# Performance work log

Measured on AMD Instinct MI355X. Metric: run time of the kernel, lower is better.

## Reference

```python
import jax, jax.numpy as jnp
import numpy as np

N_NODES = 10000
D_IN = 128
D_OUT = 128
N_EDGES = 640000


def setup_inputs() -> dict:
    key = jax.random.key(0)
    k_x, k_e, k_wl, k_wr, k_b = jax.random.split(key, 5)
    x = jax.random.normal(k_x, (N_NODES, D_IN), dtype=jnp.float32)
    edge_index = jax.random.randint(k_e, (2, N_EDGES), 0, N_NODES, dtype=jnp.int64)
    # SAGEConv params: lin_l (neighbor path, with bias), lin_r (root path, no bias)
    s_l = 1.0 / np.sqrt(D_IN)
    W_l = jax.random.uniform(k_wl, (D_OUT, D_IN), dtype=jnp.float32, minval=-s_l, maxval=s_l)
    b_l = jax.random.uniform(k_b, (D_OUT,), dtype=jnp.float32, minval=-s_l, maxval=s_l)
    W_r = jax.random.uniform(k_wr, (D_OUT, D_IN), dtype=jnp.float32, minval=-s_l, maxval=s_l)
    return {"x": x, "edge_index": edge_index, "W_l": W_l, "b_l": b_l, "W_r": W_r}


def reference(x, edge_index, W_l, b_l, W_r):
    x = x.astype(jnp.float32)
    src, dst = edge_index[0], edge_index[1]
    # gather source features, mean-aggregate into destination nodes
    msgs = x[src]                                   # [E, D_in] irregular gather
    agg_sum = jax.ops.segment_sum(msgs, dst, num_segments=N_NODES)  # [N, D_in]
    deg = jax.ops.segment_sum(jnp.ones((src.shape[0],), dtype=x.dtype), dst,
                              num_segments=N_NODES)                 # [N]
    agg = jnp.where(deg[:, None] > 0, agg_sum / jnp.maximum(deg, 1.0)[:, None], 0.0)
    # SAGEConv: lin_l(agg) + lin_r(x)
    y = agg @ W_l.T + b_l + x @ W_r.T               # [N, D_out]
    return x + y                                     # residual add
```

## Files before the change

kernel.cpp:

```cpp
#include <hip/hip_runtime.h>

#define N_NODES 10000
#define D 128
#define N_EDGES 640000
#define NB 128
#define EPB (N_EDGES / NB)
#define SB 40
#define NPSB 250

typedef __attribute__((ext_vector_type(8))) short bf16x8;
typedef __attribute__((ext_vector_type(4))) float f32x4;
typedef __attribute__((ext_vector_type(8))) unsigned short us8;
typedef __attribute__((ext_vector_type(8))) float f32x8;


__device__ __forceinline__ unsigned short f2bf(float f) {
    union { float f; unsigned int i; } v;
    v.f = f;
    unsigned int b = v.i;
    unsigned int rounded = b + 0x7fffu + ((b >> 16) & 1u);
    return (unsigned short)(rounded >> 16);
}

__device__ __forceinline__ float bf2f(unsigned short u) {
    union { unsigned int i; float f; } v;
    v.i = ((unsigned int)u) << 16;
    return v.f;
}

__device__ __forceinline__ f32x8 bf2f8(us8 v) {
    f32x8 r;
#pragma unroll
    for (int t = 0; t < 8; ++t) r[t] = bf2f(v[t]);
    return r;
}


__global__ __launch_bounds__(1024) void hist_cast_kernel(const int* __restrict__ ei,
                                                         const float4* __restrict__ x4,
                                                         const float4* __restrict__ Wl4,
                                                         const float4* __restrict__ Wr4,
                                                         ushort4* __restrict__ xh4,
                                                         ushort4* __restrict__ Wlb4,
                                                         ushort4* __restrict__ Wrb4,
                                                         unsigned short* __restrict__ lrank,
                                                         unsigned short* __restrict__ cnt,
                                                         unsigned long long* __restrict__ flags) {
    __shared__ int h[N_NODES];
    for (int n = threadIdx.x; n < N_NODES; n += 1024) h[n] = 0;
    if (blockIdx.x == 0 && threadIdx.x < SB) flags[threadIdx.x] = 0ULL;

    const int gid = blockIdx.x * 1024 + threadIdx.x;
    for (int i = gid; i < N_NODES * D / 4; i += NB * 1024) {
        float4 v = x4[i];
        ushort4 o;
        o.x = f2bf(v.x); o.y = f2bf(v.y); o.z = f2bf(v.z); o.w = f2bf(v.w);
        xh4[i] = o;
    }
    if (gid < D * D / 4) {
        float4 a = Wl4[gid], b = Wr4[gid];
        ushort4 oa, ob;
        oa.x = f2bf(a.x); oa.y = f2bf(a.y); oa.z = f2bf(a.z); oa.w = f2bf(a.w);
        ob.x = f2bf(b.x); ob.y = f2bf(b.y); ob.z = f2bf(b.z); ob.w = f2bf(b.w);
        Wlb4[gid] = oa;
        Wrb4[gid] = ob;
    }
    __syncthreads();

    const int base = blockIdx.x * EPB;
    for (int e = base + threadIdx.x; e < base + EPB; e += 1024) {
        int d = ei[N_EDGES + e];
        lrank[e] = (unsigned short)atomicAdd(&h[d], 1);
    }
    __syncthreads();
    unsigned short* c = cnt + (size_t)blockIdx.x * N_NODES;
    for (int n = threadIdx.x; n < N_NODES; n += 1024) c[n] = (unsigned short)h[n];
}


__global__ __launch_bounds__(256) void colscan_scan_kernel(unsigned short* __restrict__ cnt,
                                                           int* __restrict__ row_start,
                                                           unsigned long long* __restrict__ flags) {
    const int t = threadIdx.x;
    const int b = blockIdx.x;
    const int n = b * NPSB + t;
    __shared__ int sc[256];
    __shared__ int blk_excl_sh;

    int deg = 0;
    if (t < NPSB) {
        int s = 0;
#pragma unroll 8
        for (int j = 0; j < NB; ++j) {
            int idx = j * N_NODES + n;
            int v = cnt[idx];
            cnt[idx] = (unsigned short)s;
            s += v;
        }
        deg = s;
    }
    sc[t] = deg;
    __syncthreads();
    for (int off = 1; off < 256; off <<= 1) {
        int v = (t >= off) ? sc[t - off] : 0;
        __syncthreads();
        sc[t] += v;
        __syncthreads();
    }
    const int total = sc[255];
    const int local_excl = sc[t] - deg;

    if (t == 0) {
        int excl = 0;
        if (b == 0) {
            __hip_atomic_store(&flags[0], (2ULL << 32) | (unsigned)total,
                               __ATOMIC_RELEASE, __HIP_MEMORY_SCOPE_AGENT);
        } else {
            __hip_atomic_store(&flags[b], (1ULL << 32) | (unsigned)total,
                               __ATOMIC_RELEASE, __HIP_MEMORY_SCOPE_AGENT);
            int j = b - 1;
            while (j >= 0) {
                unsigned long long f = __hip_atomic_load(&flags[j], __ATOMIC_ACQUIRE,
                                                         __HIP_MEMORY_SCOPE_AGENT);
                unsigned st = (unsigned)(f >> 32);
                if (st == 0) continue;
                excl += (int)(unsigned)(f & 0xffffffffULL);
                if (st == 2) break;
                --j;
            }
            __hip_atomic_store(&flags[b], (2ULL << 32) | (unsigned)(excl + total),
                               __ATOMIC_RELEASE, __HIP_MEMORY_SCOPE_AGENT);
        }
        blk_excl_sh = excl;
    }
    __syncthreads();
    if (t < NPSB) row_start[n] = blk_excl_sh + local_excl;
    if (b == SB - 1 && t == 0) row_start[N_NODES] = N_EDGES;
}

__global__ __launch_bounds__(256) void scatter_kernel(const int* __restrict__ ei,
                                                      const int* __restrict__ row_start,
                                                      const unsigned short* __restrict__ cnt,
                                                      const unsigned short* __restrict__ lrank,
                                                      unsigned short* __restrict__ csr) {
    int i = blockIdx.x * 256 + threadIdx.x;
    if (i < N_EDGES) {
        int b = i / EPB;
        int s = ei[i];
        int d = ei[N_EDGES + i];
        int pos = row_start[d] + (int)cnt[b * N_NODES + d] + (int)lrank[i];
        csr[pos] = (unsigned short)s;
    }
}


__global__ __launch_bounds__(128) void aggregate_kernel(const us8* __restrict__ xh8,
                                                        const int* __restrict__ row_start,
                                                        const unsigned short* __restrict__ csr,
                                                        us8* __restrict__ aggb8) {
    __shared__ unsigned short idxs[256];
    __shared__ f32x8 red[8][16];
    const int node = blockIdx.x;
    const int lane16 = threadIdx.x & 15;
    const int slot = threadIdx.x >> 4;
    const int start = row_start[node];
    const int end = row_start[node + 1];

    f32x8 a0 = 0.f, a1 = 0.f, a2 = 0.f, a3 = 0.f;
    for (int cs = start; cs < end; cs += 256) {
        int m = min(256, end - cs);
        if ((int)threadIdx.x < m) idxs[threadIdx.x] = csr[cs + threadIdx.x];
        if ((int)threadIdx.x + 128 < m) idxs[threadIdx.x + 128] = csr[cs + threadIdx.x + 128];
        __syncthreads();
        int j = slot;
        for (; j + 24 < m; j += 32) {
            int s0 = idxs[j], s1 = idxs[j + 8], s2 = idxs[j + 16], s3 = idxs[j + 24];
            us8 v0 = xh8[s0 * 16 + lane16];
            us8 v1 = xh8[s1 * 16 + lane16];
            us8 v2 = xh8[s2 * 16 + lane16];
            us8 v3 = xh8[s3 * 16 + lane16];
            a0 += bf2f8(v0); a1 += bf2f8(v1); a2 += bf2f8(v2); a3 += bf2f8(v3);
        }
        for (; j < m; j += 8) {
            us8 v = xh8[(int)idxs[j] * 16 + lane16];
            a0 += bf2f8(v);
        }
        __syncthreads();
    }
    a0 = (a0 + a1) + (a2 + a3);
    red[slot][lane16] = a0;
    __syncthreads();
    if (slot == 0) {
        f32x8 o = red[0][lane16];
#pragma unroll
        for (int s = 1; s < 8; ++s) o += red[s][lane16];
        int cntE = end - start;
        float inv = (cntE > 0) ? 1.0f / (float)cntE : 0.0f;
        us8 pack;
#pragma unroll
        for (int t = 0; t < 8; ++t) pack[t] = f2bf(o[t] * inv);
        aggb8[node * 16 + lane16] = pack;
    }
}


__global__ __launch_bounds__(256) void lin_mfma_kernel(const float* __restrict__ x,
                                                       const unsigned short* __restrict__ aggb,
                                                       const unsigned short* __restrict__ xh,
                                                       const unsigned short* __restrict__ Wlb,
                                                       const unsigned short* __restrict__ Wrb,
                                                       const float* __restrict__ bl,
                                                       float* __restrict__ out) {
    const int wave = threadIdx.x >> 6;
    const int lane = threadIdx.x & 63;
    const int l15 = lane & 15;
    const int quad = lane >> 4;
    const int mt = blockIdx.x * 4 + wave;
    if (mt >= 625) return;
    const int row0 = mt * 16;
    const int out0 = blockIdx.y * 16;

    const int m = row0 + l15;
    const int f = out0 + l15;

    const bf16x8* arow = (const bf16x8*)(aggb + (size_t)m * D) + quad;
    const bf16x8* xrow = (const bf16x8*)(xh   + (size_t)m * D) + quad;
    const bf16x8* wlro = (const bf16x8*)(Wlb + (size_t)f * D) + quad;
    const bf16x8* wrro = (const bf16x8*)(Wrb + (size_t)f * D) + quad;

    f32x4 c = {0.f, 0.f, 0.f, 0.f};
#pragma unroll
    for (int kk = 0; kk < 4; ++kk) {
        c = __builtin_amdgcn_mfma_f32_16x16x32_bf16(arow[kk * 4], wlro[kk * 4], c, 0, 0, 0);
        c = __builtin_amdgcn_mfma_f32_16x16x32_bf16(xrow[kk * 4], wrro[kk * 4], c, 0, 0, 0);
    }

    const float bias = bl[f];
#pragma unroll
    for (int r = 0; r < 4; ++r) {
        int row = row0 + quad * 4 + r;
        int idx = row * D + f;
        out[idx] = x[idx] + bias + c[r];
    }
}

extern "C" void kernel_launch(void* const* d_in, const int* in_sizes, int n_in,
                              void* d_out, int out_size, void* d_ws, size_t ws_size,
                              hipStream_t stream) {
    const float* x  = (const float*)d_in[0];
    const int*   ei = (const int*)d_in[1];
    const float* Wl = (const float*)d_in[2];
    const float* bl = (const float*)d_in[3];
    const float* Wr = (const float*)d_in[4];
    float* out = (float*)d_out;

    unsigned long long* flags = (unsigned long long*)d_ws;
    int* row_start = (int*)(flags + 64);
    unsigned short* cnt   = (unsigned short*)(row_start + 10016);
    unsigned short* lrank = cnt + (size_t)NB * N_NODES;
    unsigned short* csr   = lrank + N_EDGES;
    unsigned short* xh    = csr + N_EDGES;
    unsigned short* aggb  = xh + (size_t)N_NODES * D;
    unsigned short* Wlb   = aggb + (size_t)N_NODES * D;
    unsigned short* Wrb   = Wlb + D * D;

    hist_cast_kernel<<<NB, 1024, 0, stream>>>(ei, (const float4*)x, (const float4*)Wl,
                                              (const float4*)Wr, (ushort4*)xh,
                                              (ushort4*)Wlb, (ushort4*)Wrb,
                                              lrank, cnt, flags);
    colscan_scan_kernel<<<SB, 256, 0, stream>>>(cnt, row_start, flags);
    scatter_kernel<<<(N_EDGES + 255) / 256, 256, 0, stream>>>(ei, row_start, cnt, lrank, csr);
    aggregate_kernel<<<N_NODES, 128, 0, stream>>>((const us8*)xh, row_start, csr,
                                                  (us8*)aggb);
    lin_mfma_kernel<<<dim3(157, 8), 256, 0, stream>>>(x, aggb, xh, Wlb, Wrb, bl, out);
}
```

Before: 121.5 us.

## Fuse all SAGE stages into one persistent kernel with grid barriers

Merges the histogram/cast, column scan, CSR scatter, mean aggregation and MFMA linear stages into a single persistent kernel of 256 blocks. The stages are separated by atomic-counter grid barriers instead of separate launches. Aggregation now maps one wave per node rather than one block per node, and reduces across slots with shuffles instead of shared memory. A memset clears the flags and barrier counter before launch. This removes launch gaps and idle tails between stages, but all blocks must be co-resident, and the per-block count array doubles in size, which makes the scan longer.

```diff
diff --git a/kernel.cpp b/kernel.cpp
--- a/kernel.cpp
+++ b/kernel.cpp
@@ -3,16 +3,17 @@
 #define N_NODES 10000
 #define D 128
 #define N_EDGES 640000
-#define NB 128
-#define EPB (N_EDGES / NB)
+#define NBLK 256
+#define NTHR 512
+#define EPB (N_EDGES / NBLK)
 #define SB 40
 #define NPSB 250
+#define NWAVES (NBLK * (NTHR / 64))
 
 typedef __attribute__((ext_vector_type(8))) short bf16x8;
 typedef __attribute__((ext_vector_type(4))) float f32x4;
 typedef __attribute__((ext_vector_type(8))) unsigned short us8;
 typedef __attribute__((ext_vector_type(8))) float f32x8;
-
 
 __device__ __forceinline__ unsigned short f2bf(float f) {
     union { float f; unsigned int i; } v;
@@ -35,212 +36,220 @@
     return r;
 }
 
-
-__global__ __launch_bounds__(1024) void hist_cast_kernel(const int* __restrict__ ei,
-                                                         const float4* __restrict__ x4,
-                                                         const float4* __restrict__ Wl4,
-                                                         const float4* __restrict__ Wr4,
-                                                         ushort4* __restrict__ xh4,
-                                                         ushort4* __restrict__ Wlb4,
-                                                         ushort4* __restrict__ Wrb4,
-                                                         unsigned short* __restrict__ lrank,
-                                                         unsigned short* __restrict__ cnt,
-                                                         unsigned long long* __restrict__ flags) {
+__device__ __forceinline__ void gbar(unsigned int* bar, unsigned int target) {
+    __syncthreads();
+    if (threadIdx.x == 0) {
+        __builtin_amdgcn_fence(__ATOMIC_RELEASE, "agent");
+        __hip_atomic_fetch_add(bar, 1u, __ATOMIC_ACQ_REL, __HIP_MEMORY_SCOPE_AGENT);
+        while (__hip_atomic_load(bar, __ATOMIC_ACQUIRE, __HIP_MEMORY_SCOPE_AGENT) < target)
+            __builtin_amdgcn_s_sleep(2);
+        __builtin_amdgcn_fence(__ATOMIC_ACQUIRE, "agent");
+    }
+    __syncthreads();
+}
+
+__global__ __launch_bounds__(NTHR) void sage_mega_kernel(
+        const float* __restrict__ x, const int* __restrict__ ei,
+        const float* __restrict__ Wl, const float* __restrict__ bl,
+        const float* __restrict__ Wr, float* __restrict__ out,
+        unsigned long long* __restrict__ flags,
+        int* __restrict__ row_start,
+        unsigned short* __restrict__ cnt,
+        unsigned short* __restrict__ lrank,
+        unsigned short* __restrict__ csr,
+        unsigned short* __restrict__ xh,
+        unsigned short* __restrict__ aggb,
+        unsigned short* __restrict__ Wlb,
+        unsigned short* __restrict__ Wrb) {
     __shared__ int h[N_NODES];
-    for (int n = threadIdx.x; n < N_NODES; n += 1024) h[n] = 0;
-    if (blockIdx.x == 0 && threadIdx.x < SB) flags[threadIdx.x] = 0ULL;
-
-    const int gid = blockIdx.x * 1024 + threadIdx.x;
-    for (int i = gid; i < N_NODES * D / 4; i += NB * 1024) {
+    unsigned int* bar = (unsigned int*)(flags + 48);
+    const int tid = threadIdx.x;
+    const int b = blockIdx.x;
+    const int gid = b * NTHR + tid;
+
+    for (int n = tid; n < N_NODES; n += NTHR) h[n] = 0;
+
+    const float4* x4 = (const float4*)x;
+    ushort4* xh4 = (ushort4*)xh;
+    for (int i = gid; i < N_NODES * D / 4; i += NBLK * NTHR) {
         float4 v = x4[i];
         ushort4 o;
         o.x = f2bf(v.x); o.y = f2bf(v.y); o.z = f2bf(v.z); o.w = f2bf(v.w);
         xh4[i] = o;
     }
     if (gid < D * D / 4) {
-        float4 a = Wl4[gid], b = Wr4[gid];
-        ushort4 oa, ob;
+        float4 a = ((const float4*)Wl)[gid], c = ((const float4*)Wr)[gid];
+        ushort4 oa, oc;
         oa.x = f2bf(a.x); oa.y = f2bf(a.y); oa.z = f2bf(a.z); oa.w = f2bf(a.w);
-        ob.x = f2bf(b.x); ob.y = f2bf(b.y); ob.z = f2bf(b.z); ob.w = f2bf(b.w);
-        Wlb4[gid] = oa;
-        Wrb4[gid] = ob;
-    }
-    __syncthreads();
-
-    const int base = blockIdx.x * EPB;
-    for (int e = base + threadIdx.x; e < base + EPB; e += 1024) {
+        oc.x = f2bf(c.x); oc.y = f2bf(c.y); oc.z = f2bf(c.z); oc.w = f2bf(c.w);
+        ((ushort4*)Wlb)[gid] = oa;
+        ((ushort4*)Wrb)[gid] = oc;
+    }
+    __syncthreads();
+
+    const int ebase = b * EPB;
+    for (int e = ebase + tid; e < ebase + EPB; e += NTHR) {
         int d = ei[N_EDGES + e];
         lrank[e] = (unsigned short)atomicAdd(&h[d], 1);
     }
     __syncthreads();
-    unsigned short* c = cnt + (size_t)blockIdx.x * N_NODES;
-    for (int n = threadIdx.x; n < N_NODES; n += 1024) c[n] = (unsigned short)h[n];
-}
-
-
-__global__ __launch_bounds__(256) void colscan_scan_kernel(unsigned short* __restrict__ cnt,
-                                                           int* __restrict__ row_start,
-                                                           unsigned long long* __restrict__ flags) {
-    const int t = threadIdx.x;
-    const int b = blockIdx.x;
-    const int n = b * NPSB + t;
-    __shared__ int sc[256];
-    __shared__ int blk_excl_sh;
-
-    int deg = 0;
-    if (t < NPSB) {
-        int s = 0;
+    {
+        unsigned short* c = cnt + (size_t)b * N_NODES;
+        for (int n = tid; n < N_NODES; n += NTHR) c[n] = (unsigned short)h[n];
+    }
+
+    gbar(bar, 1 * NBLK);
+
+    {
+        int* sc = h;
+        int deg = 0;
+        const int n = b * NPSB + tid;
+        if (b < SB && tid < NPSB) {
+            int s = 0;
 #pragma unroll 8
-        for (int j = 0; j < NB; ++j) {
-            int idx = j * N_NODES + n;
-            int v = cnt[idx];
-            cnt[idx] = (unsigned short)s;
-            s += v;
-        }
-        deg = s;
-    }
-    sc[t] = deg;
-    __syncthreads();
-    for (int off = 1; off < 256; off <<= 1) {
-        int v = (t >= off) ? sc[t - off] : 0;
-        __syncthreads();
-        sc[t] += v;
-        __syncthreads();
-    }
-    const int total = sc[255];
-    const int local_excl = sc[t] - deg;
-
-    if (t == 0) {
-        int excl = 0;
-        if (b == 0) {
-            __hip_atomic_store(&flags[0], (2ULL << 32) | (unsigned)total,
-                               __ATOMIC_RELEASE, __HIP_MEMORY_SCOPE_AGENT);
-        } else {
-            __hip_atomic_store(&flags[b], (1ULL << 32) | (unsigned)total,
-                               __ATOMIC_RELEASE, __HIP_MEMORY_SCOPE_AGENT);
-            int j = b - 1;
-            while (j >= 0) {
-                unsigned long long f = __hip_atomic_load(&flags[j], __ATOMIC_ACQUIRE,
-                                                         __HIP_MEMORY_SCOPE_AGENT);
-                unsigned st = (unsigned)(f >> 32);
-                if (st == 0) continue;
-                excl += (int)(unsigned)(f & 0xffffffffULL);
-                if (st == 2) break;
-                --j;
-            }
-            __hip_atomic_store(&flags[b], (2ULL << 32) | (unsigned)(excl + total),
-                               __ATOMIC_RELEASE, __HIP_MEMORY_SCOPE_AGENT);
-        }
-        blk_excl_sh = excl;
-    }
-    __syncthreads();
-    if (t < NPSB) row_start[n] = blk_excl_sh + local_excl;
-    if (b == SB - 1 && t == 0) row_start[N_NODES] = N_EDGES;
-}
-
-__global__ __launch_bounds__(256) void scatter_kernel(const int* __restrict__ ei,
-                                                      const int* __restrict__ row_start,
-                                                      const unsigned short* __restrict__ cnt,
-                                                      const unsigned short* __restrict__ lrank,
-                                                      unsigned short* __restrict__ csr) {
-    int i = blockIdx.x * 256 + threadIdx.x;
-    if (i < N_EDGES) {
-        int b = i / EPB;
-        int s = ei[i];
-        int d = ei[N_EDGES + i];
-        int pos = row_start[d] + (int)cnt[b * N_NODES + d] + (int)lrank[i];
-        csr[pos] = (unsigned short)s;
-    }
-}
-
-
-__global__ __launch_bounds__(128) void aggregate_kernel(const us8* __restrict__ xh8,
-                                                        const int* __restrict__ row_start,
-                                                        const unsigned short* __restrict__ csr,
-                                                        us8* __restrict__ aggb8) {
-    __shared__ unsigned short idxs[256];
-    __shared__ f32x8 red[8][16];
-    const int node = blockIdx.x;
-    const int lane16 = threadIdx.x & 15;
-    const int slot = threadIdx.x >> 4;
-    const int start = row_start[node];
-    const int end = row_start[node + 1];
-
-    f32x8 a0 = 0.f, a1 = 0.f, a2 = 0.f, a3 = 0.f;
-    for (int cs = start; cs < end; cs += 256) {
-        int m = min(256, end - cs);
-        if ((int)threadIdx.x < m) idxs[threadIdx.x] = csr[cs + threadIdx.x];
-        if ((int)threadIdx.x + 128 < m) idxs[threadIdx.x + 128] = csr[cs + threadIdx.x + 128];
-        __syncthreads();
-        int j = slot;
-        for (; j + 24 < m; j += 32) {
-            int s0 = idxs[j], s1 = idxs[j + 8], s2 = idxs[j + 16], s3 = idxs[j + 24];
-            us8 v0 = xh8[s0 * 16 + lane16];
-            us8 v1 = xh8[s1 * 16 + lane16];
-            us8 v2 = xh8[s2 * 16 + lane16];
-            us8 v3 = xh8[s3 * 16 + lane16];
-            a0 += bf2f8(v0); a1 += bf2f8(v1); a2 += bf2f8(v2); a3 += bf2f8(v3);
-        }
-        for (; j < m; j += 8) {
-            us8 v = xh8[(int)idxs[j] * 16 + lane16];
-            a0 += bf2f8(v);
-        }
-        __syncthreads();
-    }
-    a0 = (a0 + a1) + (a2 + a3);
-    red[slot][lane16] = a0;
-    __syncthreads();
-    if (slot == 0) {
-        f32x8 o = red[0][lane16];
-#pragma unroll
-        for (int s = 1; s < 8; ++s) o += red[s][lane16];
-        int cntE = end - start;
-        float inv = (cntE > 0) ? 1.0f / (float)cntE : 0.0f;
-        us8 pack;
-#pragma unroll
-        for (int t = 0; t < 8; ++t) pack[t] = f2bf(o[t] * inv);
-        aggb8[node * 16 + lane16] = pack;
-    }
-}
-
-
-__global__ __launch_bounds__(256) void lin_mfma_kernel(const float* __restrict__ x,
-                                                       const unsigned short* __restrict__ aggb,
-                                                       const unsigned short* __restrict__ xh,
-                                                       const unsigned short* __restrict__ Wlb,
-                                                       const unsigned short* __restrict__ Wrb,
-                                                       const float* __restrict__ bl,
-                                                       float* __restrict__ out) {
-    const int wave = threadIdx.x >> 6;
-    const int lane = threadIdx.x & 63;
-    const int l15 = lane & 15;
-    const int quad = lane >> 4;
-    const int mt = blockIdx.x * 4 + wave;
-    if (mt >= 625) return;
-    const int row0 = mt * 16;
-    const int out0 = blockIdx.y * 16;
-
-    const int m = row0 + l15;
-    const int f = out0 + l15;
-
-    const bf16x8* arow = (const bf16x8*)(aggb + (size_t)m * D) + quad;
-    const bf16x8* xrow = (const bf16x8*)(xh   + (size_t)m * D) + quad;
-    const bf16x8* wlro = (const bf16x8*)(Wlb + (size_t)f * D) + quad;
-    const bf16x8* wrro = (const bf16x8*)(Wrb + (size_t)f * D) + quad;
-
-    f32x4 c = {0.f, 0.f, 0.f, 0.f};
-#pragma unroll
-    for (int kk = 0; kk < 4; ++kk) {
-        c = __builtin_amdgcn_mfma_f32_16x16x32_bf16(arow[kk * 4], wlro[kk * 4], c, 0, 0, 0);
-        c = __builtin_amdgcn_mfma_f32_16x16x32_bf16(xrow[kk * 4], wrro[kk * 4], c, 0, 0, 0);
-    }
-
-    const float bias = bl[f];
-#pragma unroll
-    for (int r = 0; r < 4; ++r) {
-        int row = row0 + quad * 4 + r;
-        int idx = row * D + f;
-        out[idx] = x[idx] + bias + c[r];
+            for (int j = 0; j < NBLK; ++j) {
+                int idx = j * N_NODES + n;
+                int v = cnt[idx];
+                cnt[idx] = (unsigned short)s;
+                s += v;
+            }
+            deg = s;
+        }
+        if (b < SB) {
+            if (tid < 256) sc[tid] = (tid < NPSB) ? deg : 0;
+            __syncthreads();
+            for (int off = 1; off < 256; off <<= 1) {
+                int v = 0;
+                if (tid < 256 && tid >= off) v = sc[tid - off];
+                __syncthreads();
+                if (tid < 256) sc[tid] += v;
+                __syncthreads();
+            }
+            const int total = sc[255];
+            const int local_excl = (tid < 256) ? (sc[tid] - deg) : 0;
+            __syncthreads();
+            if (tid == 0) {
+                int excl = 0;
+                if (b == 0) {
+                    __hip_atomic_store(&flags[0], (2ULL << 32) | (unsigned)total,
+                                       __ATOMIC_RELEASE, __HIP_MEMORY_SCOPE_AGENT);
+                } else {
+                    __hip_atomic_store(&flags[b], (1ULL << 32) | (unsigned)total,
+                                       __ATOMIC_RELEASE, __HIP_MEMORY_SCOPE_AGENT);
+                    int j = b - 1;
+                    while (j >= 0) {
+                        unsigned long long f = __hip_atomic_load(&flags[j], __ATOMIC_ACQUIRE,
+                                                                 __HIP_MEMORY_SCOPE_AGENT);
+                        unsigned st = (unsigned)(f >> 32);
+                        if (st == 0) continue;
+                        excl += (int)(unsigned)(f & 0xffffffffULL);
+                        if (st == 2) break;
+                        --j;
+                    }
+                    __hip_atomic_store(&flags[b], (2ULL << 32) | (unsigned)(excl + total),
+                                       __ATOMIC_RELEASE, __HIP_MEMORY_SCOPE_AGENT);
+                }
+                sc[256] = excl;
+            }
+            __syncthreads();
+            if (tid < NPSB) row_start[n] = sc[256] + local_excl;
+            if (b == SB - 1 && tid == 0) row_start[N_NODES] = N_EDGES;
+        }
+    }
+
+    gbar(bar, 2 * NBLK);
+
+    {
+        const unsigned short* cb = cnt + (size_t)b * N_NODES;
+        for (int i = ebase + tid; i < ebase + EPB; i += NTHR) {
+            int s = ei[i];
+            int d = ei[N_EDGES + i];
+            int pos = row_start[d] + (int)cb[d] + (int)lrank[i];
+            csr[pos] = (unsigned short)s;
+        }
+    }
+
+    gbar(bar, 3 * NBLK);
+
+    {
+        const us8* xh8 = (const us8*)xh;
+        us8* aggb8 = (us8*)aggb;
+        const int wave = tid >> 6;
+        const int lane = tid & 63;
+        const int slot = lane >> 4;
+        const int lane16 = lane & 15;
+        const int gw = b * (NTHR / 64) + wave;
+
+        for (int node = gw; node < N_NODES; node += NWAVES) {
+            const int start = row_start[node];
+            const int end = row_start[node + 1];
+            f32x8 a0 = 0.f, a1 = 0.f, a2 = 0.f, a3 = 0.f;
+            int j = start + slot;
+            for (; j + 12 < end; j += 16) {
+                int i0 = csr[j], i1 = csr[j + 4], i2 = csr[j + 8], i3 = csr[j + 12];
+                us8 v0 = xh8[i0 * 16 + lane16];
+                us8 v1 = xh8[i1 * 16 + lane16];
+                us8 v2 = xh8[i2 * 16 + lane16];
+                us8 v3 = xh8[i3 * 16 + lane16];
+                a0 += bf2f8(v0); a1 += bf2f8(v1); a2 += bf2f8(v2); a3 += bf2f8(v3);
+            }
+            for (; j < end; j += 4) a0 += bf2f8(xh8[(int)csr[j] * 16 + lane16]);
+            a0 = (a0 + a1) + (a2 + a3);
+#pragma unroll
+            for (int c = 0; c < 8; ++c) {
+                float v = a0[c];
+                v += __shfl_xor(v, 16, 64);
+                v += __shfl_xor(v, 32, 64);
+                a0[c] = v;
+            }
+            if (slot == 0) {
+                int cntE = end - start;
+                float inv = (cntE > 0) ? 1.0f / (float)cntE : 0.0f;
+                us8 pack;
+#pragma unroll
+                for (int t = 0; t < 8; ++t) pack[t] = f2bf(a0[t] * inv);
+                aggb8[node * 16 + lane16] = pack;
+            }
+        }
+    }
+
+    gbar(bar, 4 * NBLK);
+
+    {
+        const int wave = tid >> 6;
+        const int lane = tid & 63;
+        const int l15 = lane & 15;
+        const int quad = lane >> 4;
+        const int gw = b * (NTHR / 64) + wave;
+
+        for (int t = gw; t < 625 * 8; t += NWAVES) {
+            const int mt = t >> 3;
+            const int ft = t & 7;
+            const int row0 = mt * 16;
+            const int out0 = ft * 16;
+            const int m = row0 + l15;
+            const int f = out0 + l15;
+
+            const bf16x8* arow = (const bf16x8*)(aggb + (size_t)m * D) + quad;
+            const bf16x8* xrow = (const bf16x8*)(xh   + (size_t)m * D) + quad;
+            const bf16x8* wlro = (const bf16x8*)(Wlb + (size_t)f * D) + quad;
+            const bf16x8* wrro = (const bf16x8*)(Wrb + (size_t)f * D) + quad;
+
+            f32x4 c = {0.f, 0.f, 0.f, 0.f};
+#pragma unroll
+            for (int kk = 0; kk < 4; ++kk) {
+                c = __builtin_amdgcn_mfma_f32_16x16x32_bf16(arow[kk * 4], wlro[kk * 4], c, 0, 0, 0);
+                c = __builtin_amdgcn_mfma_f32_16x16x32_bf16(xrow[kk * 4], wrro[kk * 4], c, 0, 0, 0);
+            }
+
+            const float bias = bl[f];
+#pragma unroll
+            for (int r = 0; r < 4; ++r) {
+                int row = row0 + quad * 4 + r;
+                int idx = row * D + f;
+                out[idx] = x[idx] + bias + c[r];
+            }
+        }
     }
 }
 
@@ -257,20 +266,16 @@
     unsigned long long* flags = (unsigned long long*)d_ws;
     int* row_start = (int*)(flags + 64);
     unsigned short* cnt   = (unsigned short*)(row_start + 10016);
-    unsigned short* lrank = cnt + (size_t)NB * N_NODES;
+    unsigned short* lrank = cnt + (size_t)NBLK * N_NODES;
     unsigned short* csr   = lrank + N_EDGES;
     unsigned short* xh    = csr + N_EDGES;
     unsigned short* aggb  = xh + (size_t)N_NODES * D;
     unsigned short* Wlb   = aggb + (size_t)N_NODES * D;
     unsigned short* Wrb   = Wlb + D * D;
 
-    hist_cast_kernel<<<NB, 1024, 0, stream>>>(ei, (const float4*)x, (const float4*)Wl,
-                                              (const float4*)Wr, (ushort4*)xh,
-                                              (ushort4*)Wlb, (ushort4*)Wrb,
-                                              lrank, cnt, flags);
-    colscan_scan_kernel<<<SB, 256, 0, stream>>>(cnt, row_start, flags);
-    scatter_kernel<<<(N_EDGES + 255) / 256, 256, 0, stream>>>(ei, row_start, cnt, lrank, csr);
-    aggregate_kernel<<<N_NODES, 128, 0, stream>>>((const us8*)xh, row_start, csr,
-                                                  (us8*)aggb);
-    lin_mfma_kernel<<<dim3(157, 8), 256, 0, stream>>>(x, aggb, xh, Wlb, Wrb, bl, out);
-}
+    (void)hipMemsetAsync(flags, 0, 512, stream);
+
+    sage_mega_kernel<<<NBLK, NTHR, 0, stream>>>(x, ei, Wl, bl, Wr, out,
+                                                flags, row_start, cnt, lrank, csr,
+                                                xh, aggb, Wlb, Wrb);
+}
```

Result: slower. 318.2 us (+161.9%).

## Fuse neighbor aggregation with MFMA linear layer and parallelize scan lookback

Applied to the files above, without the earlier changes.

Merges the aggregation and linear kernels into one, so each block aggregates 16 nodes into a shared-memory bf16 tile and then runs the MFMA projections directly, removing the aggregated-feature round trip through global memory and one launch. The histogram kernel now uses 256 blocks of 512 threads, which doubles the per-block count table the column scan has to walk. The scan's decoupled lookback is done by a whole wave with ballots instead of a serial single-thread loop. Aggregation now uses one wave per node, giving fewer blocks than before (625 versus 10000), which may reduce latency hiding on the gathers.

```diff
diff --git a/kernel.cpp b/kernel.cpp
--- a/kernel.cpp
+++ b/kernel.cpp
@@ -3,7 +3,8 @@
 #define N_NODES 10000
 #define D 128
 #define N_EDGES 640000
-#define NB 128
+#define NB 256
+#define HTHR 512
 #define EPB (N_EDGES / NB)
 #define SB 40
 #define NPSB 250
@@ -12,7 +13,6 @@
 typedef __attribute__((ext_vector_type(4))) float f32x4;
 typedef __attribute__((ext_vector_type(8))) unsigned short us8;
 typedef __attribute__((ext_vector_type(8))) float f32x8;
-
 
 __device__ __forceinline__ unsigned short f2bf(float f) {
     union { float f; unsigned int i; } v;
@@ -36,7 +36,7 @@
 }
 
 
-__global__ __launch_bounds__(1024) void hist_cast_kernel(const int* __restrict__ ei,
+__global__ __launch_bounds__(HTHR) void hist_cast_kernel(const int* __restrict__ ei,
                                                          const float4* __restrict__ x4,
                                                          const float4* __restrict__ Wl4,
                                                          const float4* __restrict__ Wr4,
@@ -47,34 +47,36 @@
                                                          unsigned short* __restrict__ cnt,
                                                          unsigned long long* __restrict__ flags) {
     __shared__ int h[N_NODES];
-    for (int n = threadIdx.x; n < N_NODES; n += 1024) h[n] = 0;
-    if (blockIdx.x == 0 && threadIdx.x < SB) flags[threadIdx.x] = 0ULL;
-
-    const int gid = blockIdx.x * 1024 + threadIdx.x;
-    for (int i = gid; i < N_NODES * D / 4; i += NB * 1024) {
+    const int tid = threadIdx.x;
+    const int b = blockIdx.x;
+    for (int n = tid; n < N_NODES; n += HTHR) h[n] = 0;
+    if (b == 0 && tid < SB) flags[tid] = 0ULL;
+
+    const int gid = b * HTHR + tid;
+    for (int i = gid; i < N_NODES * D / 4; i += NB * HTHR) {
         float4 v = x4[i];
         ushort4 o;
         o.x = f2bf(v.x); o.y = f2bf(v.y); o.z = f2bf(v.z); o.w = f2bf(v.w);
         xh4[i] = o;
     }
     if (gid < D * D / 4) {
-        float4 a = Wl4[gid], b = Wr4[gid];
-        ushort4 oa, ob;
+        float4 a = Wl4[gid], c = Wr4[gid];
+        ushort4 oa, oc;
         oa.x = f2bf(a.x); oa.y = f2bf(a.y); oa.z = f2bf(a.z); oa.w = f2bf(a.w);
-        ob.x = f2bf(b.x); ob.y = f2bf(b.y); ob.z = f2bf(b.z); ob.w = f2bf(b.w);
+        oc.x = f2bf(c.x); oc.y = f2bf(c.y); oc.z = f2bf(c.z); oc.w = f2bf(c.w);
         Wlb4[gid] = oa;
-        Wrb4[gid] = ob;
-    }
-    __syncthreads();
-
-    const int base = blockIdx.x * EPB;
-    for (int e = base + threadIdx.x; e < base + EPB; e += 1024) {
+        Wrb4[gid] = oc;
+    }
+    __syncthreads();
+
+    const int base = b * EPB;
+    for (int e = base + tid; e < base + EPB; e += HTHR) {
         int d = ei[N_EDGES + e];
         lrank[e] = (unsigned short)atomicAdd(&h[d], 1);
     }
     __syncthreads();
-    unsigned short* c = cnt + (size_t)blockIdx.x * N_NODES;
-    for (int n = threadIdx.x; n < N_NODES; n += 1024) c[n] = (unsigned short)h[n];
+    unsigned short* c = cnt + (size_t)b * N_NODES;
+    for (int n = tid; n < N_NODES; n += HTHR) c[n] = (unsigned short)h[n];
 }
 
 
@@ -84,13 +86,12 @@
     const int t = threadIdx.x;
     const int b = blockIdx.x;
     const int n = b * NPSB + t;
-    __shared__ int sc[256];
-    __shared__ int blk_excl_sh;
+    __shared__ int sc[258];
 
     int deg = 0;
     if (t < NPSB) {
         int s = 0;
-#pragma unroll 8
+#pragma unroll 16
         for (int j = 0; j < NB; ++j) {
             int idx = j * N_NODES + n;
             int v = cnt[idx];
@@ -109,34 +110,50 @@
     }
     const int total = sc[255];
     const int local_excl = sc[t] - deg;
-
-    if (t == 0) {
-        int excl = 0;
-        if (b == 0) {
+    __syncthreads();
+
+    if (b == 0) {
+        if (t == 0) {
             __hip_atomic_store(&flags[0], (2ULL << 32) | (unsigned)total,
                                __ATOMIC_RELEASE, __HIP_MEMORY_SCOPE_AGENT);
-        } else {
+            sc[256] = 0;
+        }
+    } else {
+        if (t == 0) {
             __hip_atomic_store(&flags[b], (1ULL << 32) | (unsigned)total,
                                __ATOMIC_RELEASE, __HIP_MEMORY_SCOPE_AGENT);
-            int j = b - 1;
-            while (j >= 0) {
-                unsigned long long f = __hip_atomic_load(&flags[j], __ATOMIC_ACQUIRE,
-                                                         __HIP_MEMORY_SCOPE_AGENT);
+        }
+        if (t < 64) {
+            const unsigned long long mask_b = (1ULL << b) - 1;
+            int excl;
+            for (;;) {
+                unsigned long long f = (t < b)
+                    ? __hip_atomic_load(&flags[t], __ATOMIC_ACQUIRE, __HIP_MEMORY_SCOPE_AGENT)
+                    : (2ULL << 32);
                 unsigned st = (unsigned)(f >> 32);
-                if (st == 0) continue;
-                excl += (int)(unsigned)(f & 0xffffffffULL);
-                if (st == 2) break;
-                --j;
+                unsigned long long ready = __ballot(st >= 1);
+                if ((ready & mask_b) == mask_b) {
+                    unsigned long long b2 = __ballot(st == 2) & mask_b;
+                    int j = 63 - __builtin_clzll(b2 | 1ULL);
+                    int v = (t >= j && t < b) ? (int)(unsigned)(f & 0xffffffffULL) : 0;
+#pragma unroll
+                    for (int off = 32; off > 0; off >>= 1) v += __shfl_down(v, off, 64);
+                    excl = __shfl(v, 0, 64);
+                    break;
+                }
             }
-            __hip_atomic_store(&flags[b], (2ULL << 32) | (unsigned)(excl + total),
-                               __ATOMIC_RELEASE, __HIP_MEMORY_SCOPE_AGENT);
-        }
-        blk_excl_sh = excl;
-    }
-    __syncthreads();
-    if (t < NPSB) row_start[n] = blk_excl_sh + local_excl;
+            if (t == 0) {
+                __hip_atomic_store(&flags[b], (2ULL << 32) | (unsigned)(excl + total),
+                                   __ATOMIC_RELEASE, __HIP_MEMORY_SCOPE_AGENT);
+                sc[256] = excl;
+            }
+        }
+    }
+    __syncthreads();
+    if (t < NPSB) row_start[n] = sc[256] + local_excl;
     if (b == SB - 1 && t == 0) row_start[N_NODES] = N_EDGES;
 }
+
 
 __global__ __launch_bounds__(256) void scatter_kernel(const int* __restrict__ ei,
                                                       const int* __restrict__ row_start,
@@ -148,99 +165,90 @@
         int b = i / EPB;
         int s = ei[i];
         int d = ei[N_EDGES + i];
-        int pos = row_start[d] + (int)cnt[b * N_NODES + d] + (int)lrank[i];
+        int pos = row_start[d] + (int)cnt[(size_t)b * N_NODES + d] + (int)lrank[i];
         csr[pos] = (unsigned short)s;
     }
 }
 
 
-__global__ __launch_bounds__(128) void aggregate_kernel(const us8* __restrict__ xh8,
-                                                        const int* __restrict__ row_start,
-                                                        const unsigned short* __restrict__ csr,
-                                                        us8* __restrict__ aggb8) {
-    __shared__ unsigned short idxs[256];
-    __shared__ f32x8 red[8][16];
-    const int node = blockIdx.x;
-    const int lane16 = threadIdx.x & 15;
-    const int slot = threadIdx.x >> 4;
-    const int start = row_start[node];
-    const int end = row_start[node + 1];
-
-    f32x8 a0 = 0.f, a1 = 0.f, a2 = 0.f, a3 = 0.f;
-    for (int cs = start; cs < end; cs += 256) {
-        int m = min(256, end - cs);
-        if ((int)threadIdx.x < m) idxs[threadIdx.x] = csr[cs + threadIdx.x];
-        if ((int)threadIdx.x + 128 < m) idxs[threadIdx.x + 128] = csr[cs + threadIdx.x + 128];
-        __syncthreads();
-        int j = slot;
-        for (; j + 24 < m; j += 32) {
-            int s0 = idxs[j], s1 = idxs[j + 8], s2 = idxs[j + 16], s3 = idxs[j + 24];
-            us8 v0 = xh8[s0 * 16 + lane16];
-            us8 v1 = xh8[s1 * 16 + lane16];
-            us8 v2 = xh8[s2 * 16 + lane16];
-            us8 v3 = xh8[s3 * 16 + lane16];
+__global__ __launch_bounds__(256) void agg_lin_kernel(const float* __restrict__ x,
+                                                      const unsigned short* __restrict__ xh,
+                                                      const int* __restrict__ row_start,
+                                                      const unsigned short* __restrict__ csr,
+                                                      const unsigned short* __restrict__ Wlb,
+                                                      const unsigned short* __restrict__ Wrb,
+                                                      const float* __restrict__ bl,
+                                                      float* __restrict__ out) {
+    __shared__ __align__(16) unsigned short atile[16][136];
+    const int tid = threadIdx.x;
+    const int wave = tid >> 6;
+    const int lane = tid & 63;
+    const int slot = lane >> 4;
+    const int lane16 = lane & 15;
+    const int row0 = blockIdx.x * 16;
+    const us8* xh8 = (const us8*)xh;
+
+#pragma unroll
+    for (int q = 0; q < 4; ++q) {
+        const int node = row0 + wave * 4 + q;
+        const int start = row_start[node];
+        const int end = row_start[node + 1];
+        f32x8 a0 = 0.f, a1 = 0.f, a2 = 0.f, a3 = 0.f;
+        int j = start + slot;
+        for (; j + 12 < end; j += 16) {
+            int i0 = csr[j], i1 = csr[j + 4], i2 = csr[j + 8], i3 = csr[j + 12];
+            us8 v0 = xh8[i0 * 16 + lane16];
+            us8 v1 = xh8[i1 * 16 + lane16];
+            us8 v2 = xh8[i2 * 16 + lane16];
+            us8 v3 = xh8[i3 * 16 + lane16];
             a0 += bf2f8(v0); a1 += bf2f8(v1); a2 += bf2f8(v2); a3 += bf2f8(v3);
         }
-        for (; j < m; j += 8) {
-            us8 v = xh8[(int)idxs[j] * 16 + lane16];
-            a0 += bf2f8(v);
-        }
-        __syncthreads();
-    }
-    a0 = (a0 + a1) + (a2 + a3);
-    red[slot][lane16] = a0;
-    __syncthreads();
-    if (slot == 0) {
-        f32x8 o = red[0][lane16];
-#pragma unroll
-        for (int s = 1; s < 8; ++s) o += red[s][lane16];
-        int cntE = end - start;
-        float inv = (cntE > 0) ? 1.0f / (float)cntE : 0.0f;
-        us8 pack;
-#pragma unroll
-        for (int t = 0; t < 8; ++t) pack[t] = f2bf(o[t] * inv);
-        aggb8[node * 16 + lane16] = pack;
-    }
-}
-
-
-__global__ __launch_bounds__(256) void lin_mfma_kernel(const float* __restrict__ x,
-                                                       const unsigned short* __restrict__ aggb,
-                                                       const unsigned short* __restrict__ xh,
-                                                       const unsigned short* __restrict__ Wlb,
-                                                       const unsigned short* __restrict__ Wrb,
-                                                       const float* __restrict__ bl,
-                                                       float* __restrict__ out) {
-    const int wave = threadIdx.x >> 6;
-    const int lane = threadIdx.x & 63;
+        for (; j < end; j += 4) a0 += bf2f8(xh8[(int)csr[j] * 16 + lane16]);
+        a0 = (a0 + a1) + (a2 + a3);
+#pragma unroll
+        for (int c = 0; c < 8; ++c) {
+            float v = a0[c];
+            v += __shfl_xor(v, 16, 64);
+            v += __shfl_xor(v, 32, 64);
+            a0[c] = v;
+        }
+        if (slot == 0) {
+            int cntE = end - start;
+            float inv = (cntE > 0) ? 1.0f / (float)cntE : 0.0f;
+            us8 pack;
+#pragma unroll
+            for (int t = 0; t < 8; ++t) pack[t] = f2bf(a0[t] * inv);
+            *(us8*)&atile[wave * 4 + q][lane16 * 8] = pack;
+        }
+    }
+    __syncthreads();
+
     const int l15 = lane & 15;
     const int quad = lane >> 4;
-    const int mt = blockIdx.x * 4 + wave;
-    if (mt >= 625) return;
-    const int row0 = mt * 16;
-    const int out0 = blockIdx.y * 16;
-
     const int m = row0 + l15;
-    const int f = out0 + l15;
-
-    const bf16x8* arow = (const bf16x8*)(aggb + (size_t)m * D) + quad;
-    const bf16x8* xrow = (const bf16x8*)(xh   + (size_t)m * D) + quad;
-    const bf16x8* wlro = (const bf16x8*)(Wlb + (size_t)f * D) + quad;
-    const bf16x8* wrro = (const bf16x8*)(Wrb + (size_t)f * D) + quad;
-
-    f32x4 c = {0.f, 0.f, 0.f, 0.f};
-#pragma unroll
-    for (int kk = 0; kk < 4; ++kk) {
-        c = __builtin_amdgcn_mfma_f32_16x16x32_bf16(arow[kk * 4], wlro[kk * 4], c, 0, 0, 0);
-        c = __builtin_amdgcn_mfma_f32_16x16x32_bf16(xrow[kk * 4], wrro[kk * 4], c, 0, 0, 0);
-    }
-
-    const float bias = bl[f];
-#pragma unroll
-    for (int r = 0; r < 4; ++r) {
-        int row = row0 + quad * 4 + r;
-        int idx = row * D + f;
-        out[idx] = x[idx] + bias + c[r];
+    const bf16x8* xrow = (const bf16x8*)(xh + (size_t)m * D) + quad;
+
+    for (int ft = wave; ft < 8; ft += 4) {
+        const int out0 = ft * 16;
+        const int f = out0 + l15;
+        const bf16x8* wlro = (const bf16x8*)(Wlb + (size_t)f * D) + quad;
+        const bf16x8* wrro = (const bf16x8*)(Wrb + (size_t)f * D) + quad;
+
+        f32x4 c = {0.f, 0.f, 0.f, 0.f};
+#pragma unroll
+        for (int kk = 0; kk < 4; ++kk) {
+            bf16x8 afrag = *(const bf16x8*)&atile[l15][quad * 8 + kk * 32];
+            c = __builtin_amdgcn_mfma_f32_16x16x32_bf16(afrag, wlro[kk * 4], c, 0, 0, 0);
+            c = __builtin_amdgcn_mfma_f32_16x16x32_bf16(xrow[kk * 4], wrro[kk * 4], c, 0, 0, 0);
+        }
+
+        const float bias = bl[f];
+#pragma unroll
+        for (int r = 0; r < 4; ++r) {
+            int row = row0 + quad * 4 + r;
+            int idx = row * D + f;
+            out[idx] = x[idx] + bias + c[r];
+        }
     }
 }
 
@@ -260,17 +268,15 @@
     unsigned short* lrank = cnt + (size_t)NB * N_NODES;
     unsigned short* csr   = lrank + N_EDGES;
     unsigned short* xh    = csr + N_EDGES;
-    unsigned short* aggb  = xh + (size_t)N_NODES * D;
-    unsigned short* Wlb   = aggb + (size_t)N_NODES * D;
+    unsigned short* Wlb   = xh + (size_t)N_NODES * D;
     unsigned short* Wrb   = Wlb + D * D;
 
-    hist_cast_kernel<<<NB, 1024, 0, stream>>>(ei, (const float4*)x, (const float4*)Wl,
+    hist_cast_kernel<<<NB, HTHR, 0, stream>>>(ei, (const float4*)x, (const float4*)Wl,
                                               (const float4*)Wr, (ushort4*)xh,
                                               (ushort4*)Wlb, (ushort4*)Wrb,
                                               lrank, cnt, flags);
     colscan_scan_kernel<<<SB, 256, 0, stream>>>(cnt, row_start, flags);
     scatter_kernel<<<(N_EDGES + 255) / 256, 256, 0, stream>>>(ei, row_start, cnt, lrank, csr);
-    aggregate_kernel<<<N_NODES, 128, 0, stream>>>((const us8*)xh, row_start, csr,
-                                                  (us8*)aggb);
-    lin_mfma_kernel<<<dim3(157, 8), 256, 0, stream>>>(x, aggb, xh, Wlb, Wrb, bl, out);
-}
+    agg_lin_kernel<<<N_NODES / 16, 256, 0, stream>>>(x, xh, row_start, csr,
+                                                     Wlb, Wrb, bl, out);
+}
```

Result: no change. 122.5 us (+0.9%).
